# Kernel tuning notes

Measured on AMD Instinct MI355X. Metric: run time of the kernel, lower is better.

## Reference

```python
import jax, jax.numpy as jnp
import numpy as np
import math

B, N, D, H, K = 32, 512, 768, 12, 8  # batch, patches, hidden_dim, heads, n_topic_groups
HD = D // H


def setup_inputs() -> dict:
    key = jax.random.key(0)
    ks = jax.random.split(key, 12)
    hidden_states = jax.random.normal(ks[0], (B, N, D), jnp.float32)
    # group ids in 1..K, every group present (required by original sorted-dict indexing)
    tid = jax.random.permutation(ks[1], (jnp.arange(B, dtype=jnp.int64) % K) + 1)
    s = 1.0 / math.sqrt(D)
    def lin(k):
        kw, kb = jax.random.split(k)
        return (jax.random.normal(kw, (D, D), jnp.float32) * s,
                jax.random.normal(kb, (D,), jnp.float32) * s)
    Wq, bq = lin(ks[2])
    Wk, bk = lin(ks[3])
    Wv, bv = lin(ks[4])
    Wo, bo = lin(ks[5])
    Wc, bc = lin(ks[6])  # Conv1d(D, D, kernel_size=1) == pointwise linear
    return dict(hidden_states=hidden_states, tid=tid, Wq=Wq, bq=bq, Wk=Wk, bk=bk,
                Wv=Wv, bv=bv, Wo=Wo, bo=bo, Wc=Wc, bc=bc)


def reference(hidden_states, tid, Wq, bq, Wk, bk, Wv, bv, Wo, bo, Wc, bc):
    # --- context(): per-group context_aware + mean, scattered back ---
    # context_aware(x) = mean over group of (x + conv1x1(x)); conv is pointwise so
    # it commutes with grouping -> compute per-sample then segment-mean.
    y = hidden_states + jnp.einsum('bnd,ed->bne', hidden_states, Wc) + bc  # [B,N,D]
    seg = tid - 1  # ids are 1..K
    sums = jax.ops.segment_sum(y, seg, num_segments=K)                      # [K,N,D]
    counts = jax.ops.segment_sum(jnp.ones((B,), y.dtype), seg, num_segments=K)
    means = sums / jnp.maximum(counts, 1.0)[:, None, None]
    contexts = means[seg] + hidden_states                                   # [B,N,D]

    # --- dual-stage attention (dropout rate 0 / eval mode) ---
    def heads(x):  # [B,N,D] -> [B,H,N,HD]
        return x.reshape(B, N, H, HD).transpose(0, 2, 1, 3)

    q = heads(hidden_states @ Wq.T + bq)
    t = heads(contexts @ Wq.T + bq)  # topic_states also passes through self.query
    k = heads(hidden_states @ Wk.T + bk)
    v = heads(hidden_states @ Wv.T + bv)

    scale = 1.0 / math.sqrt(HD)
    p1 = jax.nn.softmax(jnp.einsum('bhqd,bhkd->bhqk', t, k) * scale, axis=-1)
    v_t = jnp.einsum('bhqk,bhkd->bhqd', p1, v)
    p2 = jax.nn.softmax(jnp.einsum('bhqd,bhkd->bhqk', q, t) * scale, axis=-1)
    ctx = jnp.einsum('bhqk,bhkd->bhqd', p2, v_t)

    ctx = ctx.transpose(0, 2, 1, 3).reshape(B, N, D)
    return ctx @ Wo.T + bo
```

## Files before the change

kernel.cpp:

```cpp
#include <hip/hip_runtime.h>
#include <hip/hip_bf16.h>


typedef __bf16 bf16_t;
typedef __bf16 bf16x8 __attribute__((ext_vector_type(8)));
typedef __bf16 bf16x4 __attribute__((ext_vector_type(4)));
typedef float f32x4 __attribute__((ext_vector_type(4)));

#define B_ 32
#define N_ 512
#define D_ 768
#define H_ 12
#define HD_ 64
#define K_ 8
#define ND_ (N_ * D_)

typedef __attribute__((address_space(1))) unsigned int as1_u32;
typedef __attribute__((address_space(3))) unsigned int as3_u32;

__device__ __forceinline__ void glds16(const void* g, void* l) {
  __builtin_amdgcn_global_load_lds((as1_u32*)g, (as3_u32*)l, 16, 0, 0);
}

__device__ __forceinline__ f32x4 mfma16(bf16x8 a, bf16x8 b, f32x4 c) {
  return __builtin_amdgcn_mfma_f32_16x16x32_bf16(a, b, c, 0, 0, 0);
}

__device__ __forceinline__ bf16x8 addv8(bf16x8 a, bf16x8 b) {
  bf16x8 o;
#pragma unroll
  for (int j = 0; j < 8; ++j) o[j] = (bf16_t)((float)a[j] + (float)b[j]);
  return o;
}

__device__ __forceinline__ int seg_of(const int* tid, int b) {
  const bool is64 = (tid[1] == 0);
  int v = is64 ? (int)((const long long*)tid)[b] : tid[b];
  return v - 1;
}

__global__ __launch_bounds__(256) void k_cvt_all(
    const float* __restrict__ x, const float* __restrict__ Wq,
    const float* __restrict__ Wk, const float* __restrict__ Wv,
    const float* __restrict__ Wc, const float* __restrict__ Wo,
    bf16_t* __restrict__ Xb, bf16_t* __restrict__ Wqb,
    bf16_t* __restrict__ Wkb, bf16_t* __restrict__ Wvb,
    bf16_t* __restrict__ Wcb, bf16_t* __restrict__ Wob) {
  int bid = blockIdx.x;
  const float* in;
  bf16_t* out;
  if (bid < 6144) {
    in = x; out = Xb;
  } else {
    const int wi = (bid - 6144) / 288;
    bid = (bid - 6144) % 288;
    in = wi == 0 ? Wq : wi == 1 ? Wk : wi == 2 ? Wv : wi == 3 ? Wc : Wo;
    out = wi == 0 ? Wqb : wi == 1 ? Wkb : wi == 2 ? Wvb : wi == 3 ? Wcb : Wob;
  }
  const size_t i = ((size_t)bid * 256 + threadIdx.x) * 8;
  f32x4 a = *(const f32x4*)(in + i);
  f32x4 b = *(const f32x4*)(in + i + 4);
  bf16x8 o;
#pragma unroll
  for (int j = 0; j < 4; ++j) { o[j] = (bf16_t)a[j]; o[4 + j] = (bf16_t)b[j]; }
  *(bf16x8*)(out + i) = o;
}

__device__ __forceinline__ void gemm_core(const bf16_t* __restrict__ A,
                                          const bf16_t* __restrict__ Bw,
                                          char* smem, f32x4 (&acc)[4][4]) {
  const int t = threadIdx.x;
  const int lane = t & 63, w = t >> 6;
  const int quad = lane >> 4, l15 = lane & 15;
  const int r0 = t >> 2;
  const int c0e = (t & 3) * 8;
  const int wbase = w * 1024;
  const int mRow = (w >> 1) * 64, nCol = (w & 1) * 64;

  const bf16_t* ga0 = A + (size_t)r0 * D_ + c0e;
  const bf16_t* ga1 = A + (size_t)(r0 + 64) * D_ + c0e;
  const bf16_t* gb0 = Bw + (size_t)r0 * D_ + c0e;
  const bf16_t* gb1 = Bw + (size_t)(r0 + 64) * D_ + c0e;

  glds16(ga0, smem + wbase);
  glds16(ga1, smem + 4096 + wbase);
  glds16(gb0, smem + 8192 + wbase);
  glds16(gb1, smem + 12288 + wbase);

  for (int kb = 0; kb < 24; ++kb) {
    __syncthreads();
    char* cur = smem + (kb & 1) * 16384;
    char* nxt = smem + ((kb + 1) & 1) * 16384;
    if (kb < 23) {
      const int ko = (kb + 1) * 32;
      glds16(ga0 + ko, nxt + wbase);
      glds16(ga1 + ko, nxt + 4096 + wbase);
      glds16(gb0 + ko, nxt + 8192 + wbase);
      glds16(gb1 + ko, nxt + 12288 + wbase);
    }
    bf16x8 af[4], bfr[4];
#pragma unroll
    for (int mt = 0; mt < 4; ++mt)
      af[mt] = *(const bf16x8*)(cur + (mRow + mt * 16 + l15) * 64 + quad * 16);
#pragma unroll
    for (int nt = 0; nt < 4; ++nt)
      bfr[nt] = *(const bf16x8*)(cur + 8192 + (nCol + nt * 16 + l15) * 64 +
                                 quad * 16);
#pragma unroll
    for (int mt = 0; mt < 4; ++mt)
#pragma unroll
      for (int nt = 0; nt < 4; ++nt)
        acc[mt][nt] = mfma16(af[mt], bfr[nt], acc[mt][nt]);
  }
}

__device__ __forceinline__ void zero_acc(f32x4 (&acc)[4][4]) {
  const f32x4 z = {0.f, 0.f, 0.f, 0.f};
#pragma unroll
  for (int a = 0; a < 4; ++a)
#pragma unroll
    for (int b = 0; b < 4; ++b) acc[a][b] = z;
}

__global__ __launch_bounds__(256) void k_gemm_qkv(
    const bf16_t* __restrict__ X, const bf16_t* __restrict__ Wq,
    const bf16_t* __restrict__ Wk, const bf16_t* __restrict__ Wv,
    const float* __restrict__ bq, const float* __restrict__ bk,
    const float* __restrict__ bv, bf16_t* __restrict__ Q,
    bf16_t* __restrict__ Kb, bf16_t* __restrict__ V) {
  __shared__ alignas(16) char smem[32768];
  const int bid = blockIdx.x;
  const int xcd = bid & 7, i = bid >> 3;
  const int tile = i % 18, rowblk = (i / 18) * 8 + xcd;
  const int wsel = tile / 6, nb = tile % 6;
  const bf16_t* W = wsel == 0 ? Wq : wsel == 1 ? Wk : Wv;
  const float* bias = wsel == 0 ? bq : wsel == 1 ? bk : bv;
  bf16_t* Out = wsel == 0 ? Q : wsel == 1 ? Kb : V;

  f32x4 acc[4][4];
  zero_acc(acc);
  gemm_core(X + (size_t)rowblk * 128 * D_, W + (size_t)nb * 128 * D_, smem,
            acc);

  const int lane = threadIdx.x & 63, w = threadIdx.x >> 6;
  const int quad = lane >> 4, l15 = lane & 15;
  const int mbase = rowblk * 128 + (w >> 1) * 64;
  const int nbase = nb * 128 + (w & 1) * 64;
#pragma unroll
  for (int nt = 0; nt < 4; ++nt) {
    const int col = nbase + nt * 16 + l15;
    const float bb = bias[col];
#pragma unroll
    for (int mt = 0; mt < 4; ++mt)
#pragma unroll
      for (int r = 0; r < 4; ++r) {
        const int row = mbase + mt * 16 + quad * 4 + r;
        Out[(size_t)row * D_ + col] = (bf16_t)(acc[mt][nt][r] + bb);
      }
  }
}

__global__ __launch_bounds__(256) void k_gemm_plain(
    const bf16_t* __restrict__ A, const bf16_t* __restrict__ W,
    const float* __restrict__ bias, const bf16_t* __restrict__ addA,
    void* __restrict__ Out, int outF32, int swz) {
  __shared__ alignas(16) char smem[32768];
  int mblk, nblk;
  if (swz) {
    const int bid = blockIdx.x;
    const int xcd = bid & 7, i = bid >> 3;
    nblk = i % 6;
    mblk = (i / 6) * 8 + xcd;
  } else {
    mblk = blockIdx.x;
    nblk = blockIdx.y;
  }
  f32x4 acc[4][4];
  zero_acc(acc);
  gemm_core(A + (size_t)mblk * 128 * D_, W + (size_t)nblk * 128 * D_, smem,
            acc);
  const int lane = threadIdx.x & 63, w = threadIdx.x >> 6;
  const int quad = lane >> 4, l15 = lane & 15;
  const int mbase = mblk * 128 + (w >> 1) * 64;
  const int nbase = nblk * 128 + (w & 1) * 64;
#pragma unroll
  for (int nt = 0; nt < 4; ++nt) {
    const int col = nbase + nt * 16 + l15;
    const float bb = bias ? bias[col] : 0.f;
#pragma unroll
    for (int mt = 0; mt < 4; ++mt)
#pragma unroll
      for (int r = 0; r < 4; ++r) {
        const int row = mbase + mt * 16 + quad * 4 + r;
        float v = acc[mt][nt][r] + bb;
        if (addA) v += (float)addA[(size_t)row * D_ + col];
        const size_t oi = (size_t)row * D_ + col;
        if (outF32) ((float*)Out)[oi] = v;
        else ((bf16_t*)Out)[oi] = (bf16_t)v;
      }
  }
}

__global__ __launch_bounds__(256) void k_segmean(const float* __restrict__ X,
                                                 const int* __restrict__ tid,
                                                 bf16_t* __restrict__ M) {
  const size_t i = ((size_t)blockIdx.x * 256 + threadIdx.x) * 8;
  float acc[K_][8];
  float cnt[K_];
#pragma unroll
  for (int k = 0; k < K_; ++k) {
    cnt[k] = 0.f;
#pragma unroll
    for (int j = 0; j < 8; ++j) acc[k][j] = 0.f;
  }
  const bool is64 = (tid[1] == 0);
  for (int b = 0; b < B_; ++b) {
    const int s = (is64 ? (int)((const long long*)tid)[b] : tid[b]) - 1;
    const float* p = X + (size_t)b * ND_ + i;
    f32x4 y0 = *(const f32x4*)p;
    f32x4 y1 = *(const f32x4*)(p + 4);
#pragma unroll
    for (int k = 0; k < K_; ++k) {
      const float msk = (s == k) ? 1.f : 0.f;
      cnt[k] += msk;
#pragma unroll
      for (int j = 0; j < 4; ++j) {
        acc[k][j] += msk * y0[j];
        acc[k][4 + j] += msk * y1[j];
      }
    }
  }
#pragma unroll
  for (int k = 0; k < K_; ++k) {
    const float inv = 1.f / fmaxf(cnt[k], 1.f);
    bf16x8 o;
#pragma unroll
    for (int j = 0; j < 8; ++j) o[j] = (bf16_t)(acc[k][j] * inv);
    *(bf16x8*)(M + (size_t)k * ND_ + i) = o;
  }
}

__global__ __launch_bounds__(256) void k_attn(const bf16_t* __restrict__ Qp,
                                              const bf16_t* __restrict__ Kp,
                                              const bf16_t* __restrict__ Vp,
                                              const bf16_t* __restrict__ Madd,
                                              const int* __restrict__ tid,
                                              bf16_t* __restrict__ Op,
                                              int addq) {
  __shared__ alignas(16) __bf16 Kt[64][72];
  __shared__ alignas(16) __bf16 Vt[64][72];
  __shared__ alignas(16) __bf16 Pl[4][32][72];

  const int lane = threadIdx.x & 63, w = threadIdx.x >> 6;
  const int quad = lane >> 4, l15 = lane & 15;
  const int b = blockIdx.y / H_, h = blockIdx.y % H_;
  const int q0 = blockIdx.x * 128 + w * 32;
  const size_t base = (size_t)b * ND_ + h * HD_;
  const float C = 0.18033688011112042f;
  const int sg = seg_of(tid, b);
  const bf16_t* Mh = Madd + (size_t)sg * ND_ + h * HD_;

  bf16x8 aq[2][2];
#pragma unroll
  for (int mt = 0; mt < 2; ++mt)
#pragma unroll
    for (int ks = 0; ks < 2; ++ks) {
      const size_t off = (size_t)(q0 + mt * 16 + l15) * D_ + ks * 32 + quad * 8;
      bf16x8 q = *(const bf16x8*)(Qp + base + off);
      if (addq == 1) q = addv8(q, *(const bf16x8*)(Mh + off));
      aq[mt][ks] = q;
    }

  f32x4 O[2][4];
  float lacc[2][4];
  {
    const f32x4 z = {0.f, 0.f, 0.f, 0.f};
#pragma unroll
    for (int mt = 0; mt < 2; ++mt)
#pragma unroll
      for (int nt = 0; nt < 4; ++nt) O[mt][nt] = z;
#pragma unroll
    for (int mt = 0; mt < 2; ++mt)
#pragma unroll
      for (int r = 0; r < 4; ++r) lacc[mt][r] = 0.f;
  }

  const int sr = threadIdx.x >> 2, sc = threadIdx.x & 3;
  const int sig_sr = ((sr & 15) << 2) | (sr >> 4);

  bf16x8 kr[2], vr[2];
#pragma unroll
  for (int half = 0; half < 2; ++half) {
    const int cc = sc + half * 4;
    const size_t off = (size_t)sr * D_ + cc * 8;
    bf16x8 kv = *(const bf16x8*)(Kp + base + off);
    if (addq == 2) kv = addv8(kv, *(const bf16x8*)(Mh + off));
    kr[half] = kv;
    vr[half] = *(const bf16x8*)(Vp + base + off);
  }

  for (int c0 = 0; c0 < N_; c0 += 64) {
    __syncthreads();
#pragma unroll
    for (int half = 0; half < 2; ++half) {
      const int cc = sc + half * 4;
      *(bf16x8*)(&Kt[sr][cc * 8]) = kr[half];
#pragma unroll
      for (int j = 0; j < 8; ++j) Vt[cc * 8 + j][sig_sr] = vr[half][j];
    }
    __syncthreads();

    if (c0 + 64 < N_) {
#pragma unroll
      for (int half = 0; half < 2; ++half) {
        const int cc = sc + half * 4;
        const size_t off = (size_t)(c0 + 64 + sr) * D_ + cc * 8;
        bf16x8 kv = *(const bf16x8*)(Kp + base + off);
        if (addq == 2) kv = addv8(kv, *(const bf16x8*)(Mh + off));
        kr[half] = kv;
        vr[half] = *(const bf16x8*)(Vp + base + off);
      }
    }

    f32x4 S[2][4];
    {
      const f32x4 z = {0.f, 0.f, 0.f, 0.f};
#pragma unroll
      for (int mt = 0; mt < 2; ++mt)
#pragma unroll
        for (int nt = 0; nt < 4; ++nt) S[mt][nt] = z;
    }
#pragma unroll
    for (int ks = 0; ks < 2; ++ks) {
      bf16x8 bk[4];
#pragma unroll
      for (int nt = 0; nt < 4; ++nt)
        bk[nt] = *(const bf16x8*)(&Kt[nt * 16 + l15][ks * 32 + quad * 8]);
#pragma unroll
      for (int mt = 0; mt < 2; ++mt)
#pragma unroll
        for (int nt = 0; nt < 4; ++nt)
          S[mt][nt] = mfma16(aq[mt][ks], bk[nt], S[mt][nt]);
    }

#pragma unroll
    for (int mt = 0; mt < 2; ++mt)
#pragma unroll
      for (int r = 0; r < 4; ++r) {
        bf16x4 pk;
#pragma unroll
        for (int nt = 0; nt < 4; ++nt) {
          const float p = exp2f(S[mt][nt][r] * C);
          lacc[mt][r] += p;
          pk[nt] = (bf16_t)p;
        }
        *(bf16x4*)(&Pl[w][mt * 16 + quad * 4 + r][l15 * 4]) = pk;
      }

#pragma unroll
    for (int ks2 = 0; ks2 < 2; ++ks2) {
      bf16x8 ap[2], bv[4];
#pragma unroll
      for (int mt = 0; mt < 2; ++mt)
        ap[mt] = *(const bf16x8*)(&Pl[w][mt * 16 + l15][ks2 * 32 + quad * 8]);
#pragma unroll
      for (int nt2 = 0; nt2 < 4; ++nt2)
        bv[nt2] = *(const bf16x8*)(&Vt[nt2 * 16 + l15][ks2 * 32 + quad * 8]);
#pragma unroll
      for (int mt = 0; mt < 2; ++mt)
#pragma unroll
        for (int nt2 = 0; nt2 < 4; ++nt2)
          O[mt][nt2] = mfma16(ap[mt], bv[nt2], O[mt][nt2]);
    }
  }

#pragma unroll
  for (int mt = 0; mt < 2; ++mt)
#pragma unroll
    for (int r = 0; r < 4; ++r) {
      float l = lacc[mt][r];
#pragma unroll
      for (int d = 1; d < 16; d <<= 1) l += __shfl_xor(l, d);
      const float inv = 1.f / l;
      const size_t row = base + (size_t)(q0 + mt * 16 + quad * 4 + r) * D_;
#pragma unroll
      for (int nt2 = 0; nt2 < 4; ++nt2)
        Op[row + nt2 * 16 + l15] = (bf16_t)(O[mt][nt2][r] * inv);
    }
}

__global__ __launch_bounds__(256) void k_zero(float* __restrict__ out) {
  const size_t i = ((size_t)blockIdx.x * 256 + threadIdx.x) * 8;
  f32x4 z = {0.f, 0.f, 0.f, 0.f};
  *(f32x4*)(out + i) = z;
  *(f32x4*)(out + i + 4) = z;
}

extern "C" void kernel_launch(void* const* d_in, const int* in_sizes, int n_in,
                              void* d_out, int out_size, void* d_ws,
                              size_t ws_size, hipStream_t stream) {
  const float* x  = (const float*)d_in[0];
  const int*  tid = (const int*)d_in[1];
  const float* Wq = (const float*)d_in[2];
  const float* bq = (const float*)d_in[3];
  const float* Wk = (const float*)d_in[4];
  const float* bk = (const float*)d_in[5];
  const float* Wv = (const float*)d_in[6];
  const float* bv = (const float*)d_in[7];
  const float* Wo = (const float*)d_in[8];
  const float* bo = (const float*)d_in[9];
  const float* Wc = (const float*)d_in[10];
  const float* bc = (const float*)d_in[11];

  const size_t SZ  = (size_t)B_ * ND_ * sizeof(bf16_t);
  const size_t MSZ = (size_t)K_ * ND_ * sizeof(bf16_t);
  const size_t WSZ = (size_t)D_ * D_ * sizeof(bf16_t);
  if (ws_size < 3 * SZ + MSZ + 5 * WSZ) {
    k_zero<<<6144, 256, 0, stream>>>((float*)d_out);
    return;
  }

  char* ws = (char*)d_ws;
  bf16_t* Qb  = (bf16_t*)(ws);
  bf16_t* Kb  = (bf16_t*)(ws + SZ);
  bf16_t* Vb  = (bf16_t*)(ws + 2 * SZ);
  bf16_t* Mq  = (bf16_t*)(ws + 3 * SZ);
  bf16_t* Wqb = (bf16_t*)(ws + 3 * SZ + MSZ);
  bf16_t* Wkb = (bf16_t*)(ws + 3 * SZ + MSZ + WSZ);
  bf16_t* Wvb = (bf16_t*)(ws + 3 * SZ + MSZ + 2 * WSZ);
  bf16_t* Wcb = (bf16_t*)(ws + 3 * SZ + MSZ + 3 * WSZ);
  bf16_t* Wob = (bf16_t*)(ws + 3 * SZ + MSZ + 4 * WSZ);
  bf16_t* Mx = Qb;
  bf16_t* Mb = Kb;
  bf16_t* VT = (bf16_t*)d_out;
  bf16_t* Xb = (bf16_t*)d_out + (size_t)B_ * ND_;
  bf16_t* CTX = Kb;

  k_cvt_all<<<7584, 256, 0, stream>>>(x, Wq, Wk, Wv, Wc, Wo, Xb, Wqb, Wkb,
                                      Wvb, Wcb, Wob);
  k_segmean<<<192, 256, 0, stream>>>(x, tid, Mx);
  k_gemm_plain<<<dim3(32, 6), 256, 0, stream>>>(Mx, Wcb, bc, Mx, Mb, 0, 0);
  k_gemm_plain<<<dim3(32, 6), 256, 0, stream>>>(Mb, Wqb, nullptr, nullptr, Mq,
                                                0, 0);
  k_gemm_qkv<<<2304, 256, 0, stream>>>(Xb, Wqb, Wkb, Wvb, bq, bk, bv, Qb, Kb,
                                       Vb);
  k_attn<<<dim3(4, B_ * H_), 256, 0, stream>>>(Qb, Kb, Vb, Mq, tid, VT, 1);
  k_attn<<<dim3(4, B_ * H_), 256, 0, stream>>>(Qb, Qb, VT, Mq, tid, CTX, 2);
  k_gemm_plain<<<768, 256, 0, stream>>>(CTX, Wob, bo, nullptr, d_out, 1, 1);
}
```

Before: 417.9 us.

## Fuse X bf16 conversion into segmean and XOR-swizzle GEMM LDS layout

The fp32-to-bf16 conversion of the hidden states moves out of the standalone convert kernel and into the segment-mean kernel, which already reads every element of X. This removes a second full read pass over the 50MB input. The GEMM core also XOR-swizzles the 16-byte k-chunk position per row pair, both when loading into LDS and when reading fragments, to reduce LDS bank conflicts. The fused segmean kernel uses only 192 blocks, so the bf16 writes now run at low parallelism and could become a bottleneck.

```diff
diff --git a/kernel.cpp b/kernel.cpp
--- a/kernel.cpp
+++ b/kernel.cpp
@@ -39,24 +39,18 @@
   return v - 1;
 }
 
-__global__ __launch_bounds__(256) void k_cvt_all(
-    const float* __restrict__ x, const float* __restrict__ Wq,
-    const float* __restrict__ Wk, const float* __restrict__ Wv,
-    const float* __restrict__ Wc, const float* __restrict__ Wo,
-    bf16_t* __restrict__ Xb, bf16_t* __restrict__ Wqb,
+__global__ __launch_bounds__(256) void k_cvt_w(
+    const float* __restrict__ Wq, const float* __restrict__ Wk,
+    const float* __restrict__ Wv, const float* __restrict__ Wc,
+    const float* __restrict__ Wo, bf16_t* __restrict__ Wqb,
     bf16_t* __restrict__ Wkb, bf16_t* __restrict__ Wvb,
     bf16_t* __restrict__ Wcb, bf16_t* __restrict__ Wob) {
-  int bid = blockIdx.x;
-  const float* in;
-  bf16_t* out;
-  if (bid < 6144) {
-    in = x; out = Xb;
-  } else {
-    const int wi = (bid - 6144) / 288;
-    bid = (bid - 6144) % 288;
-    in = wi == 0 ? Wq : wi == 1 ? Wk : wi == 2 ? Wv : wi == 3 ? Wc : Wo;
-    out = wi == 0 ? Wqb : wi == 1 ? Wkb : wi == 2 ? Wvb : wi == 3 ? Wcb : Wob;
-  }
+  const int wi = blockIdx.x / 288;
+  const int bid = blockIdx.x % 288;
+  const float* in = wi == 0 ? Wq : wi == 1 ? Wk : wi == 2 ? Wv : wi == 3 ? Wc
+                                                                         : Wo;
+  bf16_t* out = wi == 0 ? Wqb : wi == 1 ? Wkb : wi == 2 ? Wvb : wi == 3 ? Wcb
+                                                                        : Wob;
   const size_t i = ((size_t)bid * 256 + threadIdx.x) * 8;
   f32x4 a = *(const f32x4*)(in + i);
   f32x4 b = *(const f32x4*)(in + i + 4);
@@ -73,7 +67,9 @@
   const int lane = t & 63, w = t >> 6;
   const int quad = lane >> 4, l15 = lane & 15;
   const int r0 = t >> 2;
-  const int c0e = (t & 3) * 8;
+  const int kc = (t & 3) ^ ((r0 >> 1) & 3);
+  const int c0e = kc * 8;
+  const int kcr = quad ^ ((l15 >> 1) & 3);
   const int wbase = w * 1024;
   const int mRow = (w >> 1) * 64, nCol = (w & 1) * 64;
 
@@ -101,11 +97,11 @@
     bf16x8 af[4], bfr[4];
 #pragma unroll
     for (int mt = 0; mt < 4; ++mt)
-      af[mt] = *(const bf16x8*)(cur + (mRow + mt * 16 + l15) * 64 + quad * 16);
+      af[mt] = *(const bf16x8*)(cur + (mRow + mt * 16 + l15) * 64 + kcr * 16);
 #pragma unroll
     for (int nt = 0; nt < 4; ++nt)
       bfr[nt] = *(const bf16x8*)(cur + 8192 + (nCol + nt * 16 + l15) * 64 +
-                                 quad * 16);
+                                 kcr * 16);
 #pragma unroll
     for (int mt = 0; mt < 4; ++mt)
 #pragma unroll
@@ -201,9 +197,9 @@
   }
 }
 
-__global__ __launch_bounds__(256) void k_segmean(const float* __restrict__ X,
-                                                 const int* __restrict__ tid,
-                                                 bf16_t* __restrict__ M) {
+__global__ __launch_bounds__(256) void k_segmean_cvt(
+    const float* __restrict__ X, const int* __restrict__ tid,
+    bf16_t* __restrict__ M, bf16_t* __restrict__ Xb) {
   const size_t i = ((size_t)blockIdx.x * 256 + threadIdx.x) * 8;
   float acc[K_][8];
   float cnt[K_];
@@ -219,6 +215,13 @@
     const float* p = X + (size_t)b * ND_ + i;
     f32x4 y0 = *(const f32x4*)p;
     f32x4 y1 = *(const f32x4*)(p + 4);
+    bf16x8 xb;
+#pragma unroll
+    for (int j = 0; j < 4; ++j) {
+      xb[j] = (bf16_t)y0[j];
+      xb[4 + j] = (bf16_t)y1[j];
+    }
+    *(bf16x8*)(Xb + (size_t)b * ND_ + i) = xb;
 #pragma unroll
     for (int k = 0; k < K_; ++k) {
       const float msk = (s == k) ? 1.f : 0.f;
@@ -436,9 +439,9 @@
   bf16_t* Xb = (bf16_t*)d_out + (size_t)B_ * ND_;
   bf16_t* CTX = Kb;
 
-  k_cvt_all<<<7584, 256, 0, stream>>>(x, Wq, Wk, Wv, Wc, Wo, Xb, Wqb, Wkb,
-                                      Wvb, Wcb, Wob);
-  k_segmean<<<192, 256, 0, stream>>>(x, tid, Mx);
+  k_cvt_w<<<1440, 256, 0, stream>>>(Wq, Wk, Wv, Wc, Wo, Wqb, Wkb, Wvb, Wcb,
+                                    Wob);
+  k_segmean_cvt<<<192, 256, 0, stream>>>(x, tid, Mx, Xb);
   k_gemm_plain<<<dim3(32, 6), 256, 0, stream>>>(Mx, Wcb, bc, Mx, Mb, 0, 0);
   k_gemm_plain<<<dim3(32, 6), 256, 0, stream>>>(Mb, Wqb, nullptr, nullptr, Mq,
                                                 0, 0);
```

After: 419.3 us. Within noise of the previous version (+0.4%).
